# Kernel optimization log

Hardware: AMD Instinct MI355X
Metric: run time of the kernel (lower is better)

Reference implementation:

```python
import jax, jax.numpy as jnp
import numpy as np

B, T, C, H = 8, 4096, 1024, 64

def setup_inputs() -> dict:
    key = jax.random.key(0)
    k1, k2, k3, k4 = jax.random.split(key, 4)
    return {
        "x": jax.random.normal(k1, (B, T, C), dtype=jnp.float32),
        "Wq": jax.random.normal(k2, (C, H), dtype=jnp.float32) * (C ** -0.5),
        "Wk": jax.random.normal(k3, (C, H), dtype=jnp.float32) * (C ** -0.5),
        "Wv": jax.random.normal(k4, (C, H), dtype=jnp.float32) * (C ** -0.5),
    }

def reference(x, Wq, Wk, Wv):
    # x: [B, T, C]; projections are bias-free Linears
    q = jnp.einsum("btc,ch->bth", x, Wq)  # [B, T, H]
    k = jnp.einsum("btc,ch->bth", x, Wk)
    v = jnp.einsum("btc,ch->bth", x, Wv)
    # NOTE: original scales by C**-0.5 (embed size), not head_size**-0.5
    scores = jnp.einsum("bqh,bkh->bqk", q, k) * (x.shape[-1] ** -0.5)  # [B, T, T]
    causal = jnp.tril(jnp.ones((x.shape[1], x.shape[1]), dtype=bool))
    scores = jnp.where(causal, scores, -jnp.inf)
    weights = jax.nn.softmax(scores, axis=-1)
    # dropout p=0.0 (eval) -> identity
    return jnp.einsum("bqk,bkh->bqh", weights, v)  # [B, T, H]
```

## Files before the change

### kernel.cpp

```cpp
#include <hip/hip_runtime.h>
#include <hip/hip_bf16.h>

typedef __attribute__((ext_vector_type(8))) short short8;
typedef __attribute__((ext_vector_type(4))) float f32x4;
typedef unsigned short u16;
typedef unsigned int u32;
typedef unsigned long long u64;

typedef u64    __attribute__((may_alias)) u64a;
typedef short8 __attribute__((may_alias)) short8a;
typedef float4 __attribute__((may_alias)) float4a;

#define Tseq 4096
#define LPP  72

__device__ __forceinline__ u32 pk_bf(float a, float b) {
    union { __hip_bfloat162 h; u32 u; } t;
    float2 f; f.x = a; f.y = b;
    t.h = __float22bfloat162_rn(f);
    return t.u;
}

__device__ __forceinline__ u16 f2bf(float f) {
    u32 u = __float_as_uint(f);
    u = (u + 0x7FFFu + ((u >> 16) & 1u)) >> 16;
    return (u16)u;
}

__device__ __forceinline__ short8 ld_frag_lds(const u16* p) {
    union { short8 v; u64 u[2]; } t;
    t.u[0] = *(const u64a*)(p);
    t.u[1] = *(const u64a*)(p + 4);
    return t.v;
}

__device__ __forceinline__ short8 cvt8(float4 a, float4 b) {
    union { short8 s; u32 u[4]; } t;
    t.u[0] = pk_bf(a.x, a.y); t.u[1] = pk_bf(a.z, a.w);
    t.u[2] = pk_bf(b.x, b.y); t.u[3] = pk_bf(b.z, b.w);
    return t.s;
}

__device__ __forceinline__ void gld_lds16(const void* g, void* l) {
    __builtin_amdgcn_global_load_lds(
        (const __attribute__((address_space(1))) u32*)g,
        (__attribute__((address_space(3))) u32*)l, 16, 0, 0);
}

__global__ __launch_bounds__(256) void wt_kernel(const float* __restrict__ Wq,
                                                 const float* __restrict__ Wk,
                                                 const float* __restrict__ Wv,
                                                 u16* __restrict__ wtf) {
    int idx = blockIdx.x * 256 + threadIdx.x;
    int lane = idx & 63, cc = (idx >> 6) & 31, n = (idx >> 11) & 3, mat = idx >> 13;
    const float* W = (mat == 0) ? Wq : ((mat == 1) ? Wk : Wv);
    float sc = (mat == 0) ? 0.03125f : 1.0f;
    int h = n * 16 + (lane & 15);
    int cbase = cc * 32 + (lane >> 4) * 8;
    union { short8 s; u32 u[4]; } t;
#pragma unroll
    for (int j2 = 0; j2 < 4; ++j2) {
        float a = W[(size_t)(cbase + j2 * 2)     * 64 + h] * sc;
        float b = W[(size_t)(cbase + j2 * 2 + 1) * 64 + h] * sc;
        t.u[j2] = pk_bf(a, b);
    }
    *(short8a*)(wtf + (size_t)idx * 8) = t.s;
}

__global__ __launch_bounds__(256, 2) void proj_kernel(const float* __restrict__ x,
                                                      const u16* __restrict__ wtf,
                                                      u16* __restrict__ qb,
                                                      u16* __restrict__ kA,
                                                      u16* __restrict__ vA) {
    __shared__ __align__(16) u16 Wl[2][12 * 2 * 64 * 8];

    const int tid = threadIdx.x, lane = tid & 63, wave = tid >> 6;
    const int m = lane & 15, quad = lane >> 4;
    const long rowbase = (long)blockIdx.x * 64 + wave * 16;
    const float* xr = x + (rowbase + m) * 1024 + quad * 8;

    f32x4 acc[12];
#pragma unroll
    for (int i = 0; i < 12; ++i) acc[i] = (f32x4){0.f, 0.f, 0.f, 0.f};

#define STAGE(p, buf)                                                          \
    {                                                                          \
        _Pragma("unroll")                                                      \
        for (int i = 0; i < 6; ++i) {                                          \
            int c = wave * 6 + i, mn = c >> 1, ccp = c & 1;                    \
            const u16* g = wtf + ((size_t)(mn * 32 + (p) * 2 + ccp) * 64 + lane) * 8; \
            u16* l = &Wl[buf][(size_t)(mn * 2 + ccp) * 512];                   \
            gld_lds16(g, l);                                                   \
        }                                                                      \
    }

    float4 xa[4], xb[4];
#pragma unroll
    for (int t = 0; t < 4; ++t)
        xa[t] = *(const float4a*)(xr + (t >> 1) * 32 + (t & 1) * 4);
#pragma unroll
    for (int t = 0; t < 4; ++t)
        xb[t] = *(const float4a*)(xr + (2 + (t >> 1)) * 32 + (t & 1) * 4);

    STAGE(0, 0);
    __syncthreads();

    for (int p = 0; p < 16; ++p) {
        if (p < 15) STAGE(p + 1, (p + 1) & 1);
        float4 xn[4];
        if (p < 14) {
#pragma unroll
            for (int t = 0; t < 4; ++t)
                xn[t] = *(const float4a*)(xr + (2 * (p + 2) + (t >> 1)) * 32 + (t & 1) * 4);
        }
        const u16* wb = Wl[p & 1];
#pragma unroll
        for (int ccp = 0; ccp < 2; ++ccp) {
            short8 af = cvt8(xa[ccp * 2], xa[ccp * 2 + 1]);
#pragma unroll
            for (int mn = 0; mn < 12; ++mn) {
                short8 bf = *(const short8a*)(wb + ((size_t)(mn * 2 + ccp) * 64 + lane) * 8);
                acc[mn] = __builtin_amdgcn_mfma_f32_16x16x32_bf16(af, bf, acc[mn], 0, 0, 0);
            }
        }
#pragma unroll
        for (int t = 0; t < 4; ++t) { xa[t] = xb[t]; if (p < 14) xb[t] = xn[t]; }
        __syncthreads();
    }
#undef STAGE

    const int b  = (int)(rowbase >> 12);
    const int tb = (int)(rowbase & 4095);

#pragma unroll
    for (int n = 0; n < 4; ++n)
#pragma unroll
        for (int r = 0; r < 4; ++r)
            qb[(rowbase + quad * 4 + r) * 64 + n * 16 + m] = f2bf(acc[n][r]);

#pragma unroll
    for (int n = 0; n < 4; ++n) {
        int kk = n >> 1;
        int lq = (n * 2 + (m >> 3)) & 3;
        int j  = m & 7;
#pragma unroll
        for (int r = 0; r < 4; ++r) {
            int key = tb + quad * 4 + r;
            size_t a = ((((size_t)b * 256 + (key >> 4)) * 2 + kk) * 64
                        + ((key & 15) + 16 * lq)) * 8 + j;
            kA[a] = f2bf(acc[4 + n][r]);
        }
    }

    {
        int key0 = tb + quad * 4;
        int j0 = key0 & 7;
        int q2 = (key0 >> 3) & 3;
        int kc = key0 >> 5;
#pragma unroll
        for (int n = 0; n < 4; ++n) {
            u64 pv = (u64)pk_bf(acc[8 + n][0], acc[8 + n][1])
                   | ((u64)pk_bf(acc[8 + n][2], acc[8 + n][3]) << 32);
            size_t a = ((((size_t)b * 4 + n) * 128 + kc) * 64 + (m + 16 * q2)) * 8 + j0;
            *(u64a*)(vA + a) = pv;
        }
    }
}

struct K8 { short8 k[8]; };

__device__ __forceinline__ void loadK(K8& f, const u16* kAb, int kt, int lane) {
    const u16* kp = kAb + (size_t)kt * 4096 + (size_t)lane * 8;
#pragma unroll
    for (int mt = 0; mt < 4; ++mt) {
        f.k[mt * 2]     = *(const short8a*)(kp + mt * 1024);
        f.k[mt * 2 + 1] = *(const short8a*)(kp + mt * 1024 + 512);
    }
}

__device__ __forceinline__ void loadV(short8* vf, const u16* vAb, int kt, int lane) {
    const u16* vp = vAb + (size_t)kt * 1024 + (size_t)lane * 8;
#pragma unroll
    for (int ht = 0; ht < 4; ++ht) {
        vf[ht * 2]     = *(const short8a*)(vp + (size_t)ht * 65536);
        vf[ht * 2 + 1] = *(const short8a*)(vp + (size_t)ht * 65536 + 512);
    }
}

__device__ __forceinline__ void qk_sm(const K8& f, short8 qf0, short8 qf1,
        u16* pw, float& lsum, int kt, int n_s, int qrow, int quad, int m) {
    const float L2E = 1.4426950408889634f;
    const float FMB = 4.0f * L2E;
    f32x4 s[4];
    __builtin_amdgcn_s_setprio(1);
#pragma unroll
    for (int mt = 0; mt < 4; ++mt) {
        f32x4 a = (f32x4){0.f, 0.f, 0.f, 0.f};
        a = __builtin_amdgcn_mfma_f32_16x16x32_bf16(f.k[mt * 2],     qf0, a, 0, 0, 0);
        a = __builtin_amdgcn_mfma_f32_16x16x32_bf16(f.k[mt * 2 + 1], qf1, a, 0, 0, 0);
        s[mt] = a;
    }
    __builtin_amdgcn_s_setprio(0);
    if (kt == n_s) {
#pragma unroll
        for (int mt = 0; mt < 4; ++mt)
#pragma unroll
            for (int r = 0; r < 4; ++r) {
                int key = kt * 64 + mt * 16 + quad * 4 + r;
                if (key > qrow) s[mt][r] = -1e30f;
            }
    }
#pragma unroll
    for (int mt = 0; mt < 4; ++mt) {
        float p0 = __builtin_amdgcn_exp2f(s[mt][0] * L2E - FMB);
        float p1 = __builtin_amdgcn_exp2f(s[mt][1] * L2E - FMB);
        float p2 = __builtin_amdgcn_exp2f(s[mt][2] * L2E - FMB);
        float p3 = __builtin_amdgcn_exp2f(s[mt][3] * L2E - FMB);
        lsum += (p0 + p1) + (p2 + p3);
        u64 pv = (u64)pk_bf(p0, p1) | ((u64)pk_bf(p2, p3) << 32);
        *(u64a*)(pw + m * LPP + mt * 16 + quad * 4) = pv;
    }
}

__global__ __launch_bounds__(256, 3) void attn_kernel(const u16* __restrict__ qb,
                                                      const u16* __restrict__ kA,
                                                      const u16* __restrict__ vA,
                                                      float* __restrict__ out) {
    __shared__ __align__(16) u16 Pt[4][2][16 * LPP];
    __shared__ float PubA[3][16][64];
    __shared__ float PubB[3][16][64];
    __shared__ float LA[3][64], LB[3][64];

    const int tid = threadIdx.x, lane = tid & 63, wave = tid >> 6;
    const int m = lane & 15, quad = lane >> 4;
    const int beta = blockIdx.x;
    const int b = beta & 7;
    const int u = beta >> 3;
    const int kseg = u >> 5, c = u & 31;
    const int rho = (kseg & 1) ? (kseg * 32 + 31 - c) : (kseg * 32 + c);
    const int n_s = 63 - (rho >> 1);
    const int T = n_s + 1;
    const int g = n_s * 2 + (rho & 1);
    const int qbase = g * 32;

    const int kt0 = wave * T / 4;
    const int kt1 = (wave + 1) * T / 4 - 1;

    const u16* qpA = qb + ((size_t)b * Tseq + qbase + m) * 64;
    const u16* qpB = qpA + 16 * 64;
    short8 qA0 = *(const short8a*)(qpA + quad * 8);
    short8 qA1 = *(const short8a*)(qpA + 32 + quad * 8);
    short8 qB0 = *(const short8a*)(qpB + quad * 8);
    short8 qB1 = *(const short8a*)(qpB + 32 + quad * 8);

    const u16* kAb = kA + (size_t)b * (256 * 2 * 64 * 8);
    const u16* vAb = vA + (size_t)b * (4 * 128 * 64 * 8);
    u16* pwA = Pt[wave][0];
    u16* pwB = Pt[wave][1];

    f32x4 oA[4], oB[4];
#pragma unroll
    for (int ht = 0; ht < 4; ++ht) {
        oA[ht] = (f32x4){0.f, 0.f, 0.f, 0.f};
        oB[ht] = (f32x4){0.f, 0.f, 0.f, 0.f};
    }
    float lsA = 0.f, lsB = 0.f;
    const int qrowA = qbase + m;
    const int qrowB = qbase + 16 + m;

    if (kt0 <= kt1) {
        K8 ka;
        short8 vf[8];
        loadK(ka, kAb, kt0, lane);
        for (int kt = kt0;; ++kt) {
            loadV(vf, vAb, kt, lane);
            qk_sm(ka, qA0, qA1, pwA, lsA, kt, n_s, qrowA, quad, m);
            qk_sm(ka, qB0, qB1, pwB, lsB, kt, n_s, qrowB, quad, m);
            if (kt < kt1) loadK(ka, kAb, kt + 1, lane);
            __builtin_amdgcn_wave_barrier();
            short8 pA0 = ld_frag_lds(pwA + m * LPP + quad * 8);
            short8 pA1 = ld_frag_lds(pwA + m * LPP + 32 + quad * 8);
            short8 pB0 = ld_frag_lds(pwB + m * LPP + quad * 8);
            short8 pB1 = ld_frag_lds(pwB + m * LPP + 32 + quad * 8);
            __builtin_amdgcn_s_setprio(1);
            oA[0] = __builtin_amdgcn_mfma_f32_16x16x32_bf16(vf[0], pA0, oA[0], 0, 0, 0);
            oA[0] = __builtin_amdgcn_mfma_f32_16x16x32_bf16(vf[1], pA1, oA[0], 0, 0, 0);
            oA[1] = __builtin_amdgcn_mfma_f32_16x16x32_bf16(vf[2], pA0, oA[1], 0, 0, 0);
            oA[1] = __builtin_amdgcn_mfma_f32_16x16x32_bf16(vf[3], pA1, oA[1], 0, 0, 0);
            oA[2] = __builtin_amdgcn_mfma_f32_16x16x32_bf16(vf[4], pA0, oA[2], 0, 0, 0);
            oA[2] = __builtin_amdgcn_mfma_f32_16x16x32_bf16(vf[5], pA1, oA[2], 0, 0, 0);
            oA[3] = __builtin_amdgcn_mfma_f32_16x16x32_bf16(vf[6], pA0, oA[3], 0, 0, 0);
            oA[3] = __builtin_amdgcn_mfma_f32_16x16x32_bf16(vf[7], pA1, oA[3], 0, 0, 0);
            oB[0] = __builtin_amdgcn_mfma_f32_16x16x32_bf16(vf[0], pB0, oB[0], 0, 0, 0);
            oB[0] = __builtin_amdgcn_mfma_f32_16x16x32_bf16(vf[1], pB1, oB[0], 0, 0, 0);
            oB[1] = __builtin_amdgcn_mfma_f32_16x16x32_bf16(vf[2], pB0, oB[1], 0, 0, 0);
            oB[1] = __builtin_amdgcn_mfma_f32_16x16x32_bf16(vf[3], pB1, oB[1], 0, 0, 0);
            oB[2] = __builtin_amdgcn_mfma_f32_16x16x32_bf16(vf[4], pB0, oB[2], 0, 0, 0);
            oB[2] = __builtin_amdgcn_mfma_f32_16x16x32_bf16(vf[5], pB1, oB[2], 0, 0, 0);
            oB[3] = __builtin_amdgcn_mfma_f32_16x16x32_bf16(vf[6], pB0, oB[3], 0, 0, 0);
            oB[3] = __builtin_amdgcn_mfma_f32_16x16x32_bf16(vf[7], pB1, oB[3], 0, 0, 0);
            __builtin_amdgcn_s_setprio(0);
            if (kt == kt1) break;
        }
    }

    if (wave == 0) {
#pragma unroll
        for (int ht = 0; ht < 4; ++ht) {
            PubB[0][ht * 4 + 0][lane] = oB[ht][0];
            PubB[0][ht * 4 + 1][lane] = oB[ht][1];
            PubB[0][ht * 4 + 2][lane] = oB[ht][2];
            PubB[0][ht * 4 + 3][lane] = oB[ht][3];
        }
        LB[0][lane] = lsB;
    } else if (wave == 1) {
#pragma unroll
        for (int ht = 0; ht < 4; ++ht) {
            PubA[0][ht * 4 + 0][lane] = oA[ht][0];
            PubA[0][ht * 4 + 1][lane] = oA[ht][1];
            PubA[0][ht * 4 + 2][lane] = oA[ht][2];
            PubA[0][ht * 4 + 3][lane] = oA[ht][3];
        }
        LA[0][lane] = lsA;
    } else if (wave == 2) {
#pragma unroll
        for (int ht = 0; ht < 4; ++ht) {
            PubA[1][ht * 4 + 0][lane] = oA[ht][0];
            PubA[1][ht * 4 + 1][lane] = oA[ht][1];
            PubA[1][ht * 4 + 2][lane] = oA[ht][2];
            PubA[1][ht * 4 + 3][lane] = oA[ht][3];
            PubB[1][ht * 4 + 0][lane] = oB[ht][0];
            PubB[1][ht * 4 + 1][lane] = oB[ht][1];
            PubB[1][ht * 4 + 2][lane] = oB[ht][2];
            PubB[1][ht * 4 + 3][lane] = oB[ht][3];
        }
        LA[1][lane] = lsA;
        LB[1][lane] = lsB;
    } else {
#pragma unroll
        for (int ht = 0; ht < 4; ++ht) {
            PubA[2][ht * 4 + 0][lane] = oA[ht][0];
            PubA[2][ht * 4 + 1][lane] = oA[ht][1];
            PubA[2][ht * 4 + 2][lane] = oA[ht][2];
            PubA[2][ht * 4 + 3][lane] = oA[ht][3];
            PubB[2][ht * 4 + 0][lane] = oB[ht][0];
            PubB[2][ht * 4 + 1][lane] = oB[ht][1];
            PubB[2][ht * 4 + 2][lane] = oB[ht][2];
            PubB[2][ht * 4 + 3][lane] = oB[ht][3];
        }
        LA[2][lane] = lsA;
        LB[2][lane] = lsB;
    }
    __syncthreads();

    if (wave < 2) {
        f32x4 mo[4];
        float mls;
        if (wave == 0) {
            mo[0] = oA[0]; mo[1] = oA[1]; mo[2] = oA[2]; mo[3] = oA[3];
            mls = lsA;
        } else {
            mo[0] = oB[0]; mo[1] = oB[1]; mo[2] = oB[2]; mo[3] = oB[3];
            mls = lsB;
        }
        const float (*P)[16][64] = (wave == 0) ? PubA : PubB;
        const float (*L)[64]     = (wave == 0) ? LA : LB;
#pragma unroll
        for (int j = 0; j < 3; ++j) {
#pragma unroll
            for (int ht = 0; ht < 4; ++ht) {
                mo[ht][0] += P[j][ht * 4 + 0][lane];
                mo[ht][1] += P[j][ht * 4 + 1][lane];
                mo[ht][2] += P[j][ht * 4 + 2][lane];
                mo[ht][3] += P[j][ht * 4 + 3][lane];
            }
            mls += L[j][lane];
        }

        mls += __shfl_xor(mls, 16, 64);
        mls += __shfl_xor(mls, 32, 64);
        float inv = 1.0f / mls;

        float* orow = out + ((size_t)b * Tseq + qbase + wave * 16 + m) * 64;
        float4 wv;
#pragma unroll
        for (int ht = 0; ht < 4; ++ht) {
            wv.x = mo[ht][0] * inv; wv.y = mo[ht][1] * inv;
            wv.z = mo[ht][2] * inv; wv.w = mo[ht][3] * inv;
            *(float4a*)(orow + ht * 16 + quad * 4) = wv;
        }
    }
}

extern "C" void kernel_launch(void* const* d_in, const int* in_sizes, int n_in,
                              void* d_out, int out_size, void* d_ws, size_t ws_size,
                              hipStream_t stream) {
    const float* x  = (const float*)d_in[0];
    const float* Wq = (const float*)d_in[1];
    const float* Wk = (const float*)d_in[2];
    const float* Wv = (const float*)d_in[3];
    float* out = (float*)d_out;

    char* ws = (char*)d_ws;
    u16* wtf = (u16*)ws;
    u16* qb  = (u16*)(ws + 512 * 1024);
    u16* kA  = (u16*)(ws + 512 * 1024 + 4 * 1024 * 1024);
    u16* vA  = (u16*)(ws + 512 * 1024 + 8 * 1024 * 1024);

    wt_kernel<<<96, 256, 0, stream>>>(Wq, Wk, Wv, wtf);
    proj_kernel<<<512, 256, 0, stream>>>(x, wtf, qb, kA, vA);
    attn_kernel<<<1024, 256, 0, stream>>>(qb, kA, vA, out);
}
```

Baseline: 235.6 us.

## Split attention blocks into 64-row query tiles with two-way key split

```diff
diff --git a/kernel.cpp b/kernel.cpp
--- a/kernel.cpp
+++ b/kernel.cpp
@@ -222,31 +222,32 @@
     }
 }
 
-__global__ __launch_bounds__(256, 3) void attn_kernel(const u16* __restrict__ qb,
+__global__ __launch_bounds__(256, 2) void attn_kernel(const u16* __restrict__ qb,
                                                       const u16* __restrict__ kA,
                                                       const u16* __restrict__ vA,
                                                       float* __restrict__ out) {
     __shared__ __align__(16) u16 Pt[4][2][16 * LPP];
-    __shared__ float PubA[3][16][64];
-    __shared__ float PubB[3][16][64];
-    __shared__ float LA[3][64], LB[3][64];
+    __shared__ float PubA[2][16][64];
+    __shared__ float PubB[2][16][64];
+    __shared__ float LA[2][64], LB[2][64];
 
     const int tid = threadIdx.x, lane = tid & 63, wave = tid >> 6;
     const int m = lane & 15, quad = lane >> 4;
     const int beta = blockIdx.x;
     const int b = beta & 7;
     const int u = beta >> 3;
-    const int kseg = u >> 5, c = u & 31;
-    const int rho = (kseg & 1) ? (kseg * 32 + 31 - c) : (kseg * 32 + c);
-    const int n_s = 63 - (rho >> 1);
-    const int T = n_s + 1;
-    const int g = n_s * 2 + (rho & 1);
-    const int qbase = g * 32;
-
-    const int kt0 = wave * T / 4;
-    const int kt1 = (wave + 1) * T / 4 - 1;
-
-    const u16* qpA = qb + ((size_t)b * Tseq + qbase + m) * 64;
+    const int g = 63 - u;
+    const int n_s = g;
+    const int T = g + 1;
+    const int qbase = g * 64;
+
+    const int rg = wave & 1;
+    const int hf = wave >> 1;
+    const int mid = (T + 1) >> 1;
+    const int kt0 = hf ? mid : 0;
+    const int kt1 = hf ? (T - 1) : (mid - 1);
+
+    const u16* qpA = qb + ((size_t)b * Tseq + qbase + rg * 32 + m) * 64;
     const u16* qpB = qpA + 16 * 64;
     short8 qA0 = *(const short8a*)(qpA + quad * 8);
     short8 qA1 = *(const short8a*)(qpA + 32 + quad * 8);
@@ -265,8 +266,8 @@
         oB[ht] = (f32x4){0.f, 0.f, 0.f, 0.f};
     }
     float lsA = 0.f, lsB = 0.f;
-    const int qrowA = qbase + m;
-    const int qrowB = qbase + 16 + m;
+    const int qrowA = qbase + rg * 32 + m;
+    const int qrowB = qrowA + 16;
 
     if (kt0 <= kt1) {
         K8 ka;
@@ -304,90 +305,58 @@
         }
     }
 
-    if (wave == 0) {
+    if (hf == 1) {
 #pragma unroll
         for (int ht = 0; ht < 4; ++ht) {
-            PubB[0][ht * 4 + 0][lane] = oB[ht][0];
-            PubB[0][ht * 4 + 1][lane] = oB[ht][1];
-            PubB[0][ht * 4 + 2][lane] = oB[ht][2];
-            PubB[0][ht * 4 + 3][lane] = oB[ht][3];
-        }
-        LB[0][lane] = lsB;
-    } else if (wave == 1) {
+            PubA[rg][ht * 4 + 0][lane] = oA[ht][0];
+            PubA[rg][ht * 4 + 1][lane] = oA[ht][1];
+            PubA[rg][ht * 4 + 2][lane] = oA[ht][2];
+            PubA[rg][ht * 4 + 3][lane] = oA[ht][3];
+            PubB[rg][ht * 4 + 0][lane] = oB[ht][0];
+            PubB[rg][ht * 4 + 1][lane] = oB[ht][1];
+            PubB[rg][ht * 4 + 2][lane] = oB[ht][2];
+            PubB[rg][ht * 4 + 3][lane] = oB[ht][3];
+        }
+        LA[rg][lane] = lsA;
+        LB[rg][lane] = lsB;
+    }
+    __syncthreads();
+    if (hf == 0) {
 #pragma unroll
         for (int ht = 0; ht < 4; ++ht) {
-            PubA[0][ht * 4 + 0][lane] = oA[ht][0];
-            PubA[0][ht * 4 + 1][lane] = oA[ht][1];
-            PubA[0][ht * 4 + 2][lane] = oA[ht][2];
-            PubA[0][ht * 4 + 3][lane] = oA[ht][3];
-        }
-        LA[0][lane] = lsA;
-    } else if (wave == 2) {
+            oA[ht][0] += PubA[rg][ht * 4 + 0][lane];
+            oA[ht][1] += PubA[rg][ht * 4 + 1][lane];
+            oA[ht][2] += PubA[rg][ht * 4 + 2][lane];
+            oA[ht][3] += PubA[rg][ht * 4 + 3][lane];
+            oB[ht][0] += PubB[rg][ht * 4 + 0][lane];
+            oB[ht][1] += PubB[rg][ht * 4 + 1][lane];
+            oB[ht][2] += PubB[rg][ht * 4 + 2][lane];
+            oB[ht][3] += PubB[rg][ht * 4 + 3][lane];
+        }
+        lsA += LA[rg][lane];
+        lsB += LB[rg][lane];
+
+        lsA += __shfl_xor(lsA, 16, 64);
+        lsA += __shfl_xor(lsA, 32, 64);
+        lsB += __shfl_xor(lsB, 16, 64);
+        lsB += __shfl_xor(lsB, 32, 64);
+        float invA = 1.0f / lsA;
+        float invB = 1.0f / lsB;
+
+        float* orowA = out + ((size_t)b * Tseq + qbase + rg * 32 + m) * 64;
+        float* orowB = orowA + 16 * 64;
+        float4 wv;
 #pragma unroll
         for (int ht = 0; ht < 4; ++ht) {
-            PubA[1][ht * 4 + 0][lane] = oA[ht][0];
-            PubA[1][ht * 4 + 1][lane] = oA[ht][1];
-            PubA[1][ht * 4 + 2][lane] = oA[ht][2];
-            PubA[1][ht * 4 + 3][lane] = oA[ht][3];
-            PubB[1][ht * 4 + 0][lane] = oB[ht][0];
-            PubB[1][ht * 4 + 1][lane] = oB[ht][1];
-            PubB[1][ht * 4 + 2][lane] = oB[ht][2];
-            PubB[1][ht * 4 + 3][lane] = oB[ht][3];
-        }
-        LA[1][lane] = lsA;
-        LB[1][lane] = lsB;
-    } else {
+            wv.x = oA[ht][0] * invA; wv.y = oA[ht][1] * invA;
+            wv.z = oA[ht][2] * invA; wv.w = oA[ht][3] * invA;
+            *(float4a*)(orowA + ht * 16 + quad * 4) = wv;
+        }
 #pragma unroll
         for (int ht = 0; ht < 4; ++ht) {
-            PubA[2][ht * 4 + 0][lane] = oA[ht][0];
-            PubA[2][ht * 4 + 1][lane] = oA[ht][1];
-            PubA[2][ht * 4 + 2][lane] = oA[ht][2];
-            PubA[2][ht * 4 + 3][lane] = oA[ht][3];
-            PubB[2][ht * 4 + 0][lane] = oB[ht][0];
-            PubB[2][ht * 4 + 1][lane] = oB[ht][1];
-            PubB[2][ht * 4 + 2][lane] = oB[ht][2];
-            PubB[2][ht * 4 + 3][lane] = oB[ht][3];
-        }
-        LA[2][lane] = lsA;
-        LB[2][lane] = lsB;
-    }
-    __syncthreads();
-
-    if (wave < 2) {
-        f32x4 mo[4];
-        float mls;
-        if (wave == 0) {
-            mo[0] = oA[0]; mo[1] = oA[1]; mo[2] = oA[2]; mo[3] = oA[3];
-            mls = lsA;
-        } else {
-            mo[0] = oB[0]; mo[1] = oB[1]; mo[2] = oB[2]; mo[3] = oB[3];
-            mls = lsB;
-        }
-        const float (*P)[16][64] = (wave == 0) ? PubA : PubB;
-        const float (*L)[64]     = (wave == 0) ? LA : LB;
-#pragma unroll
-        for (int j = 0; j < 3; ++j) {
-#pragma unroll
-            for (int ht = 0; ht < 4; ++ht) {
-                mo[ht][0] += P[j][ht * 4 + 0][lane];
-                mo[ht][1] += P[j][ht * 4 + 1][lane];
-                mo[ht][2] += P[j][ht * 4 + 2][lane];
-                mo[ht][3] += P[j][ht * 4 + 3][lane];
-            }
-            mls += L[j][lane];
-        }
-
-        mls += __shfl_xor(mls, 16, 64);
-        mls += __shfl_xor(mls, 32, 64);
-        float inv = 1.0f / mls;
-
-        float* orow = out + ((size_t)b * Tseq + qbase + wave * 16 + m) * 64;
-        float4 wv;
-#pragma unroll
-        for (int ht = 0; ht < 4; ++ht) {
-            wv.x = mo[ht][0] * inv; wv.y = mo[ht][1] * inv;
-            wv.z = mo[ht][2] * inv; wv.w = mo[ht][3] * inv;
-            *(float4a*)(orow + ht * 16 + quad * 4) = wv;
+            wv.x = oB[ht][0] * invB; wv.y = oB[ht][1] * invB;
+            wv.z = oB[ht][2] * invB; wv.w = oB[ht][3] * invB;
+            *(float4a*)(orowB + ht * 16 + quad * 4) = wv;
         }
     }
 }
@@ -409,5 +378,5 @@
 
     wt_kernel<<<96, 256, 0, stream>>>(Wq, Wk, Wv, wtf);
     proj_kernel<<<512, 256, 0, stream>>>(x, wtf, qb, kA, vA);
-    attn_kernel<<<1024, 256, 0, stream>>>(qb, kA, vA, out);
-}
+    attn_kernel<<<512, 256, 0, stream>>>(qb, kA, vA, out);
+}
```

New measurement: 242.7 us. 1.03x slower.
